# Kernel tuning notes

Measured on AMD Instinct MI355X. Metric: run time of the kernel, lower is better.

The kernel has to match this reference:

```python
import jax, jax.numpy as jnp
import numpy as np

D = 512          # sequence_dim
H = 8            # num_heads
DA = 64          # attn_dim per head
DV = 64          # linear_dim per head
NB = 4           # num_blocks
N = 1024         # max_seq_length + max_output_len + 1
B = 4
EPS = 1e-6


def setup_inputs() -> dict:
    key = jax.random.key(0)
    ks = jax.random.split(key, 8)
    sequence = jax.random.normal(ks[0], (B, N, D), dtype=jnp.float32)
    sequence_length = jax.random.randint(ks[1], (B,), 1, 1014)
    pos_embed = jax.random.normal(ks[2], (N, D), dtype=jnp.float32)  # nn.Embedding ~ N(0,1)
    w_uvqk = jax.random.normal(ks[3], (NB, D, 2 * H * DV + 2 * H * DA), dtype=jnp.float32) * 0.02
    w_o = jax.random.normal(ks[4], (NB, H * DV, D), dtype=jnp.float32) * 0.02
    b_o = jnp.zeros((NB, D), dtype=jnp.float32)
    ln1_g = jnp.ones((NB, D), dtype=jnp.float32)
    ln1_b = jnp.zeros((NB, D), dtype=jnp.float32)
    ln2_g = jnp.ones((NB, H * DV), dtype=jnp.float32)
    ln2_b = jnp.zeros((NB, H * DV), dtype=jnp.float32)
    pos_w = jax.random.normal(ks[5], (NB, 2 * N - 1), dtype=jnp.float32) * 0.02
    return {
        'sequence': sequence, 'sequence_length': sequence_length,
        'pos_embed': pos_embed, 'ln1_g': ln1_g, 'ln1_b': ln1_b,
        'w_uvqk': w_uvqk, 'ln2_g': ln2_g, 'ln2_b': ln2_b,
        'w_o': w_o, 'b_o': b_o, 'pos_w': pos_w,
    }


def _layer_norm(x, g, b):
    mu = jnp.mean(x, axis=-1, keepdims=True)
    var = jnp.mean(jnp.square(x - mu), axis=-1, keepdims=True)
    return (x - mu) * jax.lax.rsqrt(var + EPS) * g + b


def reference(sequence, sequence_length, pos_embed, ln1_g, ln1_b, w_uvqk,
              ln2_g, ln2_b, w_o, b_o, pos_w):
    # positional embedding + scale (inference: dropout = identity)
    x = sequence * jnp.asarray(np.sqrt(D), sequence.dtype) + pos_embed[None, :, :]
    # length mask (dense-padded equivalent of the jagged representation)
    mask = (jnp.arange(N)[None, :] < sequence_length[:, None]).astype(sequence.dtype)[..., None]
    x = x * mask
    # invalid_attn_mask = 1 - triu(ones, diag=1): causal incl. diagonal
    causal = jnp.tril(jnp.ones((N, N), sequence.dtype))
    # rel_pos_bias[i, j] = pos_w[j - i + N - 1]
    idx = jnp.arange(N)
    rel = idx[None, :] - idx[:, None] + (N - 1)  # (N, N) in [0, 2N-2]
    for l in range(NB):
        nx = _layer_norm(x, ln1_g[l], ln1_b[l])
        uvqk = jax.nn.silu(nx @ w_uvqk[l])  # (B, N, 2*H*DV + 2*H*DA)
        u, v, q, k = jnp.split(uvqk, [H * DV, 2 * H * DV, 2 * H * DV + H * DA], axis=-1)
        qh = q.reshape(x.shape[0], N, H, DA)
        kh = k.reshape(x.shape[0], N, H, DA)
        vh = v.reshape(x.shape[0], N, H, DV)
        qk = jnp.einsum('bnhd,bmhd->bhnm', qh, kh) + pos_w[l][rel][None, None]
        attn = jax.nn.silu(qk) * (causal / N)  # (B, H, N, N)
        av = jnp.einsum('bhnm,bmhd->bnhd', attn, vh).reshape(x.shape[0], N, H * DV)
        o_in = _layer_norm(av, ln2_g[l], ln2_b[l]) * u
        x = (x + o_in @ w_o[l] + b_o[l]) * mask  # mask = dense<->jagged roundtrip
    # output_embeddings[..., :D] then L2-normalize with clamped norm
    norm = jnp.linalg.norm(x, axis=-1, keepdims=True)
    return x / jnp.clip(norm, 1e-6, None)
```

## Files before the change

kernel.cpp:

```cpp
#include <hip/hip_runtime.h>
#include <math.h>
#include <stdint.h>

#define NN 1024
#define ROWS 4096
#define NBL 4

typedef _Float16 h8 __attribute__((ext_vector_type(8)));
typedef _Float16 h4 __attribute__((ext_vector_type(4)));
typedef float f4 __attribute__((ext_vector_type(4)));

__device__ __forceinline__ float fast_silu(float x) {
    float e = __builtin_amdgcn_exp2f(-1.4426950408889634f * x);
    return x * __builtin_amdgcn_rcpf(1.0f + e);
}

__device__ __forceinline__ void gl16(const void* gp, void* lp) {
    __builtin_amdgcn_global_load_lds(
        (const __attribute__((address_space(1))) uint32_t*)gp,
        (__attribute__((address_space(3))) uint32_t*)lp, 16, 0, 0);
}

__device__ __forceinline__ float wred(float s) {
    #pragma unroll
    for (int off = 1; off < 64; off <<= 1) s += __shfl_xor(s, off);
    return s;
}

__global__ __launch_bounds__(256) void k_transpose16(const float* __restrict__ wuvqk,
                                                     _Float16* __restrict__ wuT,
                                                     const float* __restrict__ wo,
                                                     _Float16* __restrict__ woT) {
    __shared__ _Float16 T[64][66];
    int z = blockIdx.z;
    const float* s; _Float16* d; int N;
    if (z < 4) { N = 2048; s = wuvqk + (size_t)z * 512 * 2048; d = wuT + (size_t)z * 2048 * 512; }
    else {
        if (blockIdx.x >= 8) return;
        N = 512; s = wo + (size_t)(z - 4) * 512 * 512; d = woT + (size_t)(z - 4) * 512 * 512;
    }
    int n0 = blockIdx.x << 6, k0 = blockIdx.y << 6;
    int tx = threadIdx.x & 63, ty = threadIdx.x >> 6;
    #pragma unroll
    for (int q = 0; q < 16; ++q)
        T[(q << 2) + ty][tx] = (_Float16)s[(size_t)(k0 + (q << 2) + ty) * N + n0 + tx];
    __syncthreads();
    #pragma unroll
    for (int q = 0; q < 16; ++q)
        d[(size_t)(n0 + (q << 2) + ty) * 512 + k0 + tx] = T[tx][(q << 2) + ty];
}

template<int MODE>
__global__ __launch_bounds__(256) void k_lnw(const float* __restrict__ X,
                                             const float* __restrict__ X2,
                                             const float* __restrict__ X3,
                                             const float* __restrict__ seq,
                                             const float* __restrict__ pos,
                                             const int* __restrict__ slen,
                                             const float* __restrict__ g,
                                             const float* __restrict__ bt,
                                             _Float16* __restrict__ O,
                                             const _Float16* __restrict__ U,
                                             float* __restrict__ Xw) {
    int tid = threadIdx.x;
    int w = tid >> 6, lane = tid & 63;
    int c = lane << 3;
    #pragma unroll
    for (int rr = 0; rr < 2; ++rr) {
        int row = (blockIdx.x << 3) + (w << 1) + rr;
        float v[8];
        if (MODE == 1) {
            int b = row >> 10, n = row & (NN - 1);
            float m = (n < slen[b]) ? 1.0f : 0.0f;
            const float4* sp = (const float4*)&seq[(size_t)row * 512 + c];
            const float4* pp = (const float4*)&pos[(size_t)n * 512 + c];
            const float SD = 22.627416997969522f;
            float4 s0 = sp[0], s1 = sp[1], p0 = pp[0], p1 = pp[1];
            v[0]=(s0.x*SD+p0.x)*m; v[1]=(s0.y*SD+p0.y)*m; v[2]=(s0.z*SD+p0.z)*m; v[3]=(s0.w*SD+p0.w)*m;
            v[4]=(s1.x*SD+p1.x)*m; v[5]=(s1.y*SD+p1.y)*m; v[6]=(s1.z*SD+p1.z)*m; v[7]=(s1.w*SD+p1.w)*m;
            float4 o0, o1;
            o0.x=v[0]; o0.y=v[1]; o0.z=v[2]; o0.w=v[3];
            o1.x=v[4]; o1.y=v[5]; o1.z=v[6]; o1.w=v[7];
            float4* xp = (float4*)&Xw[(size_t)row * 512 + c];
            xp[0] = o0; xp[1] = o1;
        } else {
            const float4* xp = (const float4*)&X[(size_t)row * 512 + c];
            float4 a = xp[0], b4 = xp[1];
            v[0]=a.x; v[1]=a.y; v[2]=a.z; v[3]=a.w; v[4]=b4.x; v[5]=b4.y; v[6]=b4.z; v[7]=b4.w;
            if (MODE == 2) {
                int nn = row & (NN - 1);
                if (nn >= 384) {
                    const float4* qp = (const float4*)&X2[(size_t)row * 512 + c];
                    float4 t0 = qp[0], t1 = qp[1];
                    v[0]+=t0.x; v[1]+=t0.y; v[2]+=t0.z; v[3]+=t0.w;
                    v[4]+=t1.x; v[5]+=t1.y; v[6]+=t1.z; v[7]+=t1.w;
                }
                if (nn >= 768) {
                    const float4* qp = (const float4*)&X3[(size_t)row * 512 + c];
                    float4 t0 = qp[0], t1 = qp[1];
                    v[0]+=t0.x; v[1]+=t0.y; v[2]+=t0.z; v[3]+=t0.w;
                    v[4]+=t1.x; v[5]+=t1.y; v[6]+=t1.z; v[7]+=t1.w;
                }
            }
        }
        float s = v[0]+v[1]+v[2]+v[3]+v[4]+v[5]+v[6]+v[7];
        s = wred(s);
        float mu = s * (1.0f / 512.0f);
        float ss = 0.0f;
        #pragma unroll
        for (int i = 0; i < 8; ++i) { float d = v[i] - mu; ss += d * d; }
        ss = wred(ss);
        float rs = rsqrtf(ss * (1.0f / 512.0f) + 1e-6f);

        const float4* gp = (const float4*)&g[c];
        const float4* bp = (const float4*)&bt[c];
        float4 g0 = gp[0], g1 = gp[1], b0 = bp[0], b1 = bp[1];
        float gg[8] = {g0.x,g0.y,g0.z,g0.w,g1.x,g1.y,g1.z,g1.w};
        float bb[8] = {b0.x,b0.y,b0.z,b0.w,b1.x,b1.y,b1.z,b1.w};
        float o[8];
        #pragma unroll
        for (int i = 0; i < 8; ++i) o[i] = (v[i] - mu) * rs * gg[i] + bb[i];
        if (MODE == 2) {
            h8 uu = *(const h8*)&U[(size_t)row * 2048 + c];
            #pragma unroll
            for (int i = 0; i < 8; ++i) o[i] *= (float)uu[i];
        }
        h8 oh;
        #pragma unroll
        for (int i = 0; i < 8; ++i) oh[i] = (_Float16)o[i];
        *(h8*)&O[(size_t)row * 512 + c] = oh;
    }
}

__global__ __launch_bounds__(256) void k_normw(float* __restrict__ X) {
    int tid = threadIdx.x;
    int w = tid >> 6, lane = tid & 63;
    int c = lane << 3;
    #pragma unroll
    for (int rr = 0; rr < 2; ++rr) {
        int row = (blockIdx.x << 3) + (w << 1) + rr;
        float4* xp = (float4*)&X[(size_t)row * 512 + c];
        float4 a = xp[0], b4 = xp[1];
        float ss = a.x*a.x + a.y*a.y + a.z*a.z + a.w*a.w +
                   b4.x*b4.x + b4.y*b4.y + b4.z*b4.z + b4.w*b4.w;
        ss = wred(ss);
        float sc = 1.0f / fmaxf(sqrtf(ss), 1e-6f);
        a.x*=sc; a.y*=sc; a.z*=sc; a.w*=sc; b4.x*=sc; b4.y*=sc; b4.z*=sc; b4.w*=sc;
        xp[0] = a; xp[1] = b4;
    }
}

template<int EPI, int BM, int BN, int WAVES, int WGR, int WGC>
__global__ __launch_bounds__(WAVES * 64) void k_gemm(const _Float16* __restrict__ A,
                                                     const _Float16* __restrict__ Bm,
                                                     _Float16* __restrict__ Cu,
                                                     _Float16* __restrict__ vT,
                                                     const float* __restrict__ bo,
                                                     const int* __restrict__ slen,
                                                     float* __restrict__ Xio) {
    constexpr int WR = BM / WGR / 16;
    constexpr int WC = BN / WGC / 16;
    constexpr int QA = BM * 8 / (WAVES * 64);
    constexpr int QB = BN * 8 / (WAVES * 64);
    __shared__ _Float16 smem[2 * 64 * (BM + BN)];
    _Float16* AsB = smem;
    _Float16* BsB = smem + 2 * BM * 64;
    int tid = threadIdx.x;
    int w = tid >> 6, lane = tid & 63;
    int t = lane & 15, gq = lane >> 4;
    int flat = blockIdx.y * gridDim.x + blockIdx.x;
    int cpx = (gridDim.x * gridDim.y) >> 3;
    int f2 = (flat & 7) * cpx + (flat >> 3);
    int bx = f2 % gridDim.x, by = f2 / gridDim.x;
    int row0 = by * BM, col0 = bx * BN;
    int wr = (w / WGC) * (BM / WGR), wc = (w % WGC) * (BN / WGC);

    f4 zero4 = {0.0f, 0.0f, 0.0f, 0.0f};
    f4 acc[WR][WC];
    #pragma unroll
    for (int i = 0; i < WR; ++i)
        #pragma unroll
        for (int j = 0; j < WC; ++j) acc[i][j] = zero4;

    auto stage = [&](int buf, int k0) {
        _Float16* As = AsB + buf * BM * 64;
        _Float16* Bs = BsB + buf * BN * 64;
        #pragma unroll
        for (int q = 0; q < QA; ++q) {
            int s = (q * WAVES + w) * 64 + lane;
            int r = s >> 3, cs = (s & 7) ^ (r & 7);
            gl16(A + (size_t)(row0 + r) * 512 + k0 + (cs << 3),
                 (char*)As + (size_t)(q * WAVES + w) * 1024);
        }
        #pragma unroll
        for (int q = 0; q < QB; ++q) {
            int s = (q * WAVES + w) * 64 + lane;
            int r = s >> 3, cs = (s & 7) ^ (r & 7);
            gl16(Bm + (size_t)(col0 + r) * 512 + k0 + (cs << 3),
                 (char*)Bs + (size_t)(q * WAVES + w) * 1024);
        }
    };

    stage(0, 0);
    int cur = 0;
    for (int k0 = 0; k0 < 512; k0 += 64) {
        __syncthreads();
        if (k0 + 64 < 512) stage(cur ^ 1, k0 + 64);
        const char* As = (const char*)(AsB + cur * BM * 64);
        const char* Bs = (const char*)(BsB + cur * BN * 64);
        h8 af[WR][2], bf[WC][2];
        #pragma unroll
        for (int i = 0; i < WR; ++i) {
            int rl = wr + (i << 4) + t;
            #pragma unroll
            for (int ks = 0; ks < 2; ++ks)
                af[i][ks] = *(const h8*)(As + rl * 128 + (((gq + (ks << 2)) ^ (rl & 7)) << 4));
        }
        #pragma unroll
        for (int j = 0; j < WC; ++j) {
            int nl = wc + (j << 4) + t;
            #pragma unroll
            for (int ks = 0; ks < 2; ++ks)
                bf[j][ks] = *(const h8*)(Bs + nl * 128 + (((gq + (ks << 2)) ^ (nl & 7)) << 4));
        }
        #pragma unroll
        for (int i = 0; i < WR; ++i)
            #pragma unroll
            for (int j = 0; j < WC; ++j) {
                acc[i][j] = __builtin_amdgcn_mfma_f32_16x16x32_f16(af[i][0], bf[j][0], acc[i][j], 0, 0, 0);
                acc[i][j] = __builtin_amdgcn_mfma_f32_16x16x32_f16(af[i][1], bf[j][1], acc[i][j], 0, 0, 0);
            }
        cur ^= 1;
    }

    if (EPI == 0) {
        _Float16* E = smem;
        bool vblk = (col0 >= 512 && col0 < 1024);
        __syncthreads();
        if (vblk) {
            #pragma unroll
            for (int i = 0; i < WR; ++i)
                #pragma unroll
                for (int j = 0; j < WC; ++j) {
                    int cl = wc + (j << 4) + t;
                    int rl = wr + (i << 4) + (gq << 2);
                    h4 pk;
                    #pragma unroll
                    for (int rr = 0; rr < 4; ++rr) pk[rr] = (_Float16)fast_silu(acc[i][j][rr]);
                    *(h4*)&E[cl * 136 + rl] = pk;
                }
        } else {
            #pragma unroll
            for (int i = 0; i < WR; ++i)
                #pragma unroll
                for (int j = 0; j < WC; ++j) {
                    int cl = wc + (j << 4) + t;
                    int rl = wr + (i << 4) + (gq << 2);
                    #pragma unroll
                    for (int rr = 0; rr < 4; ++rr)
                        E[(rl + rr) * 136 + cl] = (_Float16)fast_silu(acc[i][j][rr]);
                }
        }
        __syncthreads();
        constexpr int ITERS = 128 * 16 / (WAVES * 64);
        if (vblk) {
            int b = row0 >> 10;
            int n0l = row0 & 1023;
            #pragma unroll
            for (int it = 0; it < ITERS; ++it) {
                int dl = it * (WAVES * 4) + (tid >> 4);
                int cc = tid & 15;
                h8 vv = *(const h8*)&E[dl * 136 + (cc << 3)];
                int hh = (col0 + dl - 512) >> 6, dd = (col0 + dl - 512) & 63;
                *(h8*)&vT[((size_t)((b << 3) + hh) * 64 + dd) * 1024 + n0l + (cc << 3)] = vv;
            }
        } else {
            #pragma unroll
            for (int it = 0; it < ITERS; ++it) {
                int rl = it * (WAVES * 4) + (tid >> 4);
                int cc = tid & 15;
                h8 vv = *(const h8*)&E[rl * 136 + (cc << 3)];
                *(h8*)&Cu[(size_t)(row0 + rl) * 2048 + col0 + (cc << 3)] = vv;
            }
        }
    } else {
        #pragma unroll
        for (int i = 0; i < WR; ++i) {
            #pragma unroll
            for (int j = 0; j < WC; ++j) {
                int colf = col0 + wc + (j << 4) + t;
                int rowb = row0 + wr + (i << 4) + (gq << 2);
                int b = rowb >> 10;
                #pragma unroll
                for (int rr = 0; rr < 4; ++rr) {
                    int row = rowb + rr;
                    float m = ((row & 1023) < slen[b]) ? 1.0f : 0.0f;
                    size_t ix = (size_t)row * 512 + colf;
                    Xio[ix] = (Xio[ix] + acc[i][j][rr] + bo[colf]) * m;
                }
            }
        }
    }
}

__global__ __launch_bounds__(256) void k_attn(const _Float16* __restrict__ uvqk,
                                              const _Float16* __restrict__ vT,
                                              const float* __restrict__ posw,
                                              float* __restrict__ av0,
                                              float* __restrict__ av1,
                                              float* __restrict__ av2) {
    __shared__ _Float16 Ks[2][64 * 64];
    __shared__ _Float16 Vs[64 * 64];
    __shared__ _Float16 Ps[64 * 72];
    __shared__ float pws[2][128];
    int tid = threadIdx.x;
    int w = tid >> 6, lane = tid & 63;
    int t = lane & 15, gq = lane >> 4;
    int flat = blockIdx.x + 30 * (blockIdx.y + 8 * blockIdx.z);
    int f2 = (flat & 7) * 120 + (flat >> 3);
    int u = f2 % 30, h = (f2 / 30) & 7, b = f2 / 240;

    int nt, mlo, mhi;
    float* avout;
    if (u < 6) { nt = u; mlo = 0; mhi = nt; avout = av0; }
    else if (u < 18) {
        int p = u - 6; nt = 6 + (p >> 1);
        int c0 = (nt + 2) >> 1;
        if (p & 1) { mlo = c0; mhi = nt; avout = av1; }
        else       { mlo = 0;  mhi = c0 - 1; avout = av0; }
    } else {
        int p = u - 18; int third = p / 3; nt = 12 + third; int q3 = p - 3 * third;
        int c = nt + 1, c1 = (c + 2) / 3, c2 = (2 * c + 2) / 3;
        if (q3 == 0)      { mlo = 0;  mhi = c1 - 1; avout = av0; }
        else if (q3 == 1) { mlo = c1; mhi = c2 - 1; avout = av1; }
        else              { mlo = c2; mhi = nt;     avout = av2; }
    }
    int n0 = nt << 6;

    const _Float16* qbase = uvqk + (size_t)b * NN * 2048 + 1024 + h * 64;
    const _Float16* kbase = uvqk + (size_t)b * NN * 2048 + 1536 + h * 64;
    const _Float16* vbase = vT + (size_t)((b << 3) + h) * 64 * 1024;

    #pragma unroll
    for (int q = 0; q < 2; ++q) {
        int s = (((w << 1) + q) << 6) + lane;
        int r = s >> 3, cs = (s & 7) ^ (r & 7);
        gl16(qbase + (size_t)(n0 + r) * 2048 + (cs << 3),
             (char*)&Ks[1][0] + (size_t)(((w << 1) + q) << 6) * 16);
        gl16(kbase + (size_t)((mlo << 6) + r) * 2048 + (cs << 3),
             (char*)&Ks[0][0] + (size_t)(((w << 1) + q) << 6) * 16);
    }
    if (tid < 128) pws[0][tid] = posw[(mlo << 6) - n0 + tid + 960];
    __syncthreads();

    h8 aq[2];
    {
        int rl = (w << 4) + t;
        #pragma unroll
        for (int ks = 0; ks < 2; ++ks)
            aq[ks] = *(const h8*)((const char*)&Ks[1][0] + rl * 128 +
                                  (((gq + (ks << 2)) ^ (rl & 7)) << 4));
    }
    asm volatile("s_waitcnt lgkmcnt(0)" ::: "memory");
    __builtin_amdgcn_sched_barrier(0);
    __syncthreads();

    f4 zero4 = {0.0f, 0.0f, 0.0f, 0.0f};
    f4 avacc[4];
    #pragma unroll
    for (int j = 0; j < 4; ++j) avacc[j] = zero4;

    int cur = 0;
    for (int mt = mlo; mt <= mhi; ++mt) {
        int m0 = mt << 6;
        #pragma unroll
        for (int q = 0; q < 2; ++q) {
            int s = (((w << 1) + q) << 6) + lane;
            int r = s >> 3, cs = (s & 7) ^ (r & 7);
            gl16(vbase + (size_t)r * 1024 + m0 + (cs << 3),
                 (char*)&Vs[0] + (size_t)(((w << 1) + q) << 6) * 16);
        }
        int mt2 = (mt < mhi) ? mt + 1 : mt;
        #pragma unroll
        for (int q = 0; q < 2; ++q) {
            int s = (((w << 1) + q) << 6) + lane;
            int r = s >> 3, cs = (s & 7) ^ (r & 7);
            gl16(kbase + (size_t)((mt2 << 6) + r) * 2048 + (cs << 3),
                 (char*)&Ks[cur ^ 1][0] + (size_t)(((w << 1) + q) << 6) * 16);
        }
        if (tid < 128) pws[cur ^ 1][tid] = posw[(mt2 << 6) - n0 + tid + 960];

        f4 sacc[4];
        __builtin_amdgcn_s_setprio(1);
        #pragma unroll
        for (int i = 0; i < 4; ++i) {
            f4 binit;
            #pragma unroll
            for (int rr = 0; rr < 4; ++rr)
                binit[rr] = pws[cur][63 + (i << 4) + (gq << 2) + rr - ((w << 4) + t)];
            int ml = (i << 4) + t;
            h8 ak0 = *(const h8*)((const char*)&Ks[cur][0] + ml * 128 + (((gq + 0) ^ (ml & 7)) << 4));
            h8 ak1 = *(const h8*)((const char*)&Ks[cur][0] + ml * 128 + (((gq + 4) ^ (ml & 7)) << 4));
            sacc[i] = __builtin_amdgcn_mfma_f32_16x16x32_f16(ak0, aq[0], binit, 0, 0, 0);
            sacc[i] = __builtin_amdgcn_mfma_f32_16x16x32_f16(ak1, aq[1], sacc[i], 0, 0, 0);
        }
        __builtin_amdgcn_s_setprio(0);
        int nabs = n0 + (w << 4) + t;
        #pragma unroll
        for (int i = 0; i < 4; ++i) {
            int mb = m0 + (i << 4) + (gq << 2);
            h4 pk;
            #pragma unroll
            for (int rr = 0; rr < 4; ++rr) {
                float p = (mb + rr <= nabs) ? fast_silu(sacc[i][rr]) : 0.0f;
                pk[rr] = (_Float16)p;
            }
            *(h4*)((char*)Ps + ((w << 4) + t) * 144 + (i << 5) + (gq << 3)) = pk;
        }
        asm volatile("s_waitcnt lgkmcnt(0)" ::: "memory");
        asm volatile("s_waitcnt vmcnt(2)" ::: "memory");
        __builtin_amdgcn_s_barrier();
        __builtin_amdgcn_s_setprio(1);
        #pragma unroll
        for (int ks = 0; ks < 2; ++ks) {
            h8 pa = *(const h8*)((const char*)Ps + ((w << 4) + t) * 144 + (ks << 6) + (gq << 4));
            #pragma unroll
            for (int jt = 0; jt < 4; ++jt) {
                int dl = (jt << 4) + t;
                h8 bv = *(const h8*)((const char*)&Vs[0] + dl * 128 +
                                     (((gq + (ks << 2)) ^ (dl & 7)) << 4));
                avacc[jt] = __builtin_amdgcn_mfma_f32_16x16x32_f16(pa, bv, avacc[jt], 0, 0, 0);
            }
        }
        __builtin_amdgcn_s_setprio(0);
        __syncthreads();
        cur ^= 1;
    }

    #pragma unroll
    for (int jt = 0; jt < 4; ++jt) {
        #pragma unroll
        for (int rr = 0; rr < 4; ++rr) {
            int n = n0 + (w << 4) + (gq << 2) + rr;
            int d = (jt << 4) + t;
            avout[(size_t)(b * NN + n) * 512 + h * 64 + d] = avacc[jt][rr] * (1.0f / 1024.0f);
        }
    }
}

extern "C" void kernel_launch(void* const* d_in, const int* in_sizes, int n_in,
                              void* d_out, int out_size, void* d_ws, size_t ws_size,
                              hipStream_t stream) {
    const float* seq   = (const float*)d_in[0];
    const int*   slen  = (const int*)d_in[1];
    const float* pos   = (const float*)d_in[2];
    const float* ln1g  = (const float*)d_in[3];
    const float* ln1b  = (const float*)d_in[4];
    const float* wuvqk = (const float*)d_in[5];
    const float* ln2g  = (const float*)d_in[6];
    const float* ln2b  = (const float*)d_in[7];
    const float* wo    = (const float*)d_in[8];
    const float* bo    = (const float*)d_in[9];
    const float* posw  = (const float*)d_in[10];

    float* x = (float*)d_out;
    char* W = (char*)d_ws;
    _Float16* nx16   = (_Float16*)(W);
    _Float16* oin16  = (_Float16*)(W + (4u << 20));
    _Float16* uvqk16 = (_Float16*)(W + (8u << 20));
    _Float16* vT16   = (_Float16*)(W + (24u << 20));
    float*    av0    = (float*)   (W + (28u << 20));
    float*    av1    = (float*)   (W + (36u << 20));
    float*    av2    = (float*)   (W + (44u << 20));
    _Float16* wuT16  = (_Float16*)(W + (52u << 20));
    _Float16* woT16  = (_Float16*)(W + (60u << 20));

    k_transpose16<<<dim3(32, 8, 8), 256, 0, stream>>>(wuvqk, wuT16, wo, woT16);
    for (int l = 0; l < NBL; ++l) {
        if (l == 0)
            k_lnw<1><<<512, 256, 0, stream>>>(nullptr, nullptr, nullptr, seq, pos, slen,
                                              ln1g, ln1b, nx16, nullptr, x);
        else
            k_lnw<0><<<512, 256, 0, stream>>>(x, nullptr, nullptr, nullptr, nullptr, nullptr,
                                              ln1g + l * 512, ln1b + l * 512, nx16, nullptr, nullptr);
        k_gemm<0, 128, 128, 8, 2, 4><<<dim3(16, 32), 512, 0, stream>>>(
            nx16, wuT16 + (size_t)l * 2048 * 512, uvqk16, vT16, nullptr, nullptr, nullptr);
        k_attn<<<dim3(30, 8, NBL), 256, 0, stream>>>(uvqk16, vT16, posw + l * (2 * NN - 1),
                                                     av0, av1, av2);
        k_lnw<2><<<512, 256, 0, stream>>>(av0, av1, av2, nullptr, nullptr, nullptr,
                                          ln2g + l * 512, ln2b + l * 512, oin16, uvqk16, nullptr);
        k_gemm<1, 64, 32, 4, 2, 2><<<dim3(16, 64), 256, 0, stream>>>(
            oin16, woT16 + (size_t)l * 512 * 512, nullptr, nullptr, bo + l * 512, slen, x);
    }
    k_normw<<<512, 256, 0, stream>>>(x);
}
```

Before: 208.7 us.

## Fuse second layernorm and u-gating into output projection GEMM

```diff
diff --git a/kernel.cpp b/kernel.cpp
--- a/kernel.cpp
+++ b/kernel.cpp
@@ -52,15 +52,12 @@
 
 template<int MODE>
 __global__ __launch_bounds__(256) void k_lnw(const float* __restrict__ X,
-                                             const float* __restrict__ X2,
-                                             const float* __restrict__ X3,
                                              const float* __restrict__ seq,
                                              const float* __restrict__ pos,
                                              const int* __restrict__ slen,
                                              const float* __restrict__ g,
                                              const float* __restrict__ bt,
                                              _Float16* __restrict__ O,
-                                             const _Float16* __restrict__ U,
                                              float* __restrict__ Xw) {
     int tid = threadIdx.x;
     int w = tid >> 6, lane = tid & 63;
@@ -87,21 +84,6 @@
             const float4* xp = (const float4*)&X[(size_t)row * 512 + c];
             float4 a = xp[0], b4 = xp[1];
             v[0]=a.x; v[1]=a.y; v[2]=a.z; v[3]=a.w; v[4]=b4.x; v[5]=b4.y; v[6]=b4.z; v[7]=b4.w;
-            if (MODE == 2) {
-                int nn = row & (NN - 1);
-                if (nn >= 384) {
-                    const float4* qp = (const float4*)&X2[(size_t)row * 512 + c];
-                    float4 t0 = qp[0], t1 = qp[1];
-                    v[0]+=t0.x; v[1]+=t0.y; v[2]+=t0.z; v[3]+=t0.w;
-                    v[4]+=t1.x; v[5]+=t1.y; v[6]+=t1.z; v[7]+=t1.w;
-                }
-                if (nn >= 768) {
-                    const float4* qp = (const float4*)&X3[(size_t)row * 512 + c];
-                    float4 t0 = qp[0], t1 = qp[1];
-                    v[0]+=t0.x; v[1]+=t0.y; v[2]+=t0.z; v[3]+=t0.w;
-                    v[4]+=t1.x; v[5]+=t1.y; v[6]+=t1.z; v[7]+=t1.w;
-                }
-            }
         }
         float s = v[0]+v[1]+v[2]+v[3]+v[4]+v[5]+v[6]+v[7];
         s = wred(s);
@@ -117,17 +99,9 @@
         float4 g0 = gp[0], g1 = gp[1], b0 = bp[0], b1 = bp[1];
         float gg[8] = {g0.x,g0.y,g0.z,g0.w,g1.x,g1.y,g1.z,g1.w};
         float bb[8] = {b0.x,b0.y,b0.z,b0.w,b1.x,b1.y,b1.z,b1.w};
-        float o[8];
-        #pragma unroll
-        for (int i = 0; i < 8; ++i) o[i] = (v[i] - mu) * rs * gg[i] + bb[i];
-        if (MODE == 2) {
-            h8 uu = *(const h8*)&U[(size_t)row * 2048 + c];
-            #pragma unroll
-            for (int i = 0; i < 8; ++i) o[i] *= (float)uu[i];
-        }
         h8 oh;
         #pragma unroll
-        for (int i = 0; i < 8; ++i) oh[i] = (_Float16)o[i];
+        for (int i = 0; i < 8; ++i) oh[i] = (_Float16)((v[i] - mu) * rs * gg[i] + bb[i]);
         *(h8*)&O[(size_t)row * 512 + c] = oh;
     }
 }
@@ -150,18 +124,12 @@
     }
 }
 
-template<int EPI, int BM, int BN, int WAVES, int WGR, int WGC>
-__global__ __launch_bounds__(WAVES * 64) void k_gemm(const _Float16* __restrict__ A,
-                                                     const _Float16* __restrict__ Bm,
-                                                     _Float16* __restrict__ Cu,
-                                                     _Float16* __restrict__ vT,
-                                                     const float* __restrict__ bo,
-                                                     const int* __restrict__ slen,
-                                                     float* __restrict__ Xio) {
-    constexpr int WR = BM / WGR / 16;
-    constexpr int WC = BN / WGC / 16;
-    constexpr int QA = BM * 8 / (WAVES * 64);
-    constexpr int QB = BN * 8 / (WAVES * 64);
+__global__ __launch_bounds__(512) void k_gemm0(const _Float16* __restrict__ A,
+                                               const _Float16* __restrict__ Bm,
+                                               _Float16* __restrict__ Cu,
+                                               _Float16* __restrict__ vT) {
+    constexpr int BM = 128, BN = 128, WAVES = 8;
+    constexpr int QA = 2, QB = 2;
     __shared__ _Float16 smem[2 * 64 * (BM + BN)];
     _Float16* AsB = smem;
     _Float16* BsB = smem + 2 * BM * 64;
@@ -173,14 +141,14 @@
     int f2 = (flat & 7) * cpx + (flat >> 3);
     int bx = f2 % gridDim.x, by = f2 / gridDim.x;
     int row0 = by * BM, col0 = bx * BN;
-    int wr = (w / WGC) * (BM / WGR), wc = (w % WGC) * (BN / WGC);
+    int wr = (w >> 2) << 6, wc = (w & 3) << 5;
 
     f4 zero4 = {0.0f, 0.0f, 0.0f, 0.0f};
-    f4 acc[WR][WC];
-    #pragma unroll
-    for (int i = 0; i < WR; ++i)
-        #pragma unroll
-        for (int j = 0; j < WC; ++j) acc[i][j] = zero4;
+    f4 acc[4][2];
+    #pragma unroll
+    for (int i = 0; i < 4; ++i)
+        #pragma unroll
+        for (int j = 0; j < 2; ++j) acc[i][j] = zero4;
 
     auto stage = [&](int buf, int k0) {
         _Float16* As = AsB + buf * BM * 64;
@@ -208,97 +176,77 @@
         if (k0 + 64 < 512) stage(cur ^ 1, k0 + 64);
         const char* As = (const char*)(AsB + cur * BM * 64);
         const char* Bs = (const char*)(BsB + cur * BN * 64);
-        h8 af[WR][2], bf[WC][2];
-        #pragma unroll
-        for (int i = 0; i < WR; ++i) {
+        h8 af[4][2], bf[2][2];
+        #pragma unroll
+        for (int i = 0; i < 4; ++i) {
             int rl = wr + (i << 4) + t;
             #pragma unroll
             for (int ks = 0; ks < 2; ++ks)
                 af[i][ks] = *(const h8*)(As + rl * 128 + (((gq + (ks << 2)) ^ (rl & 7)) << 4));
         }
         #pragma unroll
-        for (int j = 0; j < WC; ++j) {
+        for (int j = 0; j < 2; ++j) {
             int nl = wc + (j << 4) + t;
             #pragma unroll
             for (int ks = 0; ks < 2; ++ks)
                 bf[j][ks] = *(const h8*)(Bs + nl * 128 + (((gq + (ks << 2)) ^ (nl & 7)) << 4));
         }
         #pragma unroll
-        for (int i = 0; i < WR; ++i)
-            #pragma unroll
-            for (int j = 0; j < WC; ++j) {
+        for (int i = 0; i < 4; ++i)
+            #pragma unroll
+            for (int j = 0; j < 2; ++j) {
                 acc[i][j] = __builtin_amdgcn_mfma_f32_16x16x32_f16(af[i][0], bf[j][0], acc[i][j], 0, 0, 0);
                 acc[i][j] = __builtin_amdgcn_mfma_f32_16x16x32_f16(af[i][1], bf[j][1], acc[i][j], 0, 0, 0);
             }
         cur ^= 1;
     }
 
-    if (EPI == 0) {
-        _Float16* E = smem;
-        bool vblk = (col0 >= 512 && col0 < 1024);
-        __syncthreads();
-        if (vblk) {
-            #pragma unroll
-            for (int i = 0; i < WR; ++i)
+    _Float16* E = smem;
+    bool vblk = (col0 >= 512 && col0 < 1024);
+    __syncthreads();
+    if (vblk) {
+        #pragma unroll
+        for (int i = 0; i < 4; ++i)
+            #pragma unroll
+            for (int j = 0; j < 2; ++j) {
+                int cl = wc + (j << 4) + t;
+                int rl = wr + (i << 4) + (gq << 2);
+                h4 pk;
                 #pragma unroll
-                for (int j = 0; j < WC; ++j) {
-                    int cl = wc + (j << 4) + t;
-                    int rl = wr + (i << 4) + (gq << 2);
-                    h4 pk;
-                    #pragma unroll
-                    for (int rr = 0; rr < 4; ++rr) pk[rr] = (_Float16)fast_silu(acc[i][j][rr]);
-                    *(h4*)&E[cl * 136 + rl] = pk;
-                }
-        } else {
-            #pragma unroll
-            for (int i = 0; i < WR; ++i)
+                for (int rr = 0; rr < 4; ++rr) pk[rr] = (_Float16)fast_silu(acc[i][j][rr]);
+                *(h4*)&E[cl * 136 + rl] = pk;
+            }
+    } else {
+        #pragma unroll
+        for (int i = 0; i < 4; ++i)
+            #pragma unroll
+            for (int j = 0; j < 2; ++j) {
+                int cl = wc + (j << 4) + t;
+                int rl = wr + (i << 4) + (gq << 2);
                 #pragma unroll
-                for (int j = 0; j < WC; ++j) {
-                    int cl = wc + (j << 4) + t;
-                    int rl = wr + (i << 4) + (gq << 2);
-                    #pragma unroll
-                    for (int rr = 0; rr < 4; ++rr)
-                        E[(rl + rr) * 136 + cl] = (_Float16)fast_silu(acc[i][j][rr]);
-                }
-        }
-        __syncthreads();
-        constexpr int ITERS = 128 * 16 / (WAVES * 64);
-        if (vblk) {
-            int b = row0 >> 10;
-            int n0l = row0 & 1023;
-            #pragma unroll
-            for (int it = 0; it < ITERS; ++it) {
-                int dl = it * (WAVES * 4) + (tid >> 4);
-                int cc = tid & 15;
-                h8 vv = *(const h8*)&E[dl * 136 + (cc << 3)];
-                int hh = (col0 + dl - 512) >> 6, dd = (col0 + dl - 512) & 63;
-                *(h8*)&vT[((size_t)((b << 3) + hh) * 64 + dd) * 1024 + n0l + (cc << 3)] = vv;
+                for (int rr = 0; rr < 4; ++rr)
+                    E[(rl + rr) * 136 + cl] = (_Float16)fast_silu(acc[i][j][rr]);
             }
-        } else {
-            #pragma unroll
-            for (int it = 0; it < ITERS; ++it) {
-                int rl = it * (WAVES * 4) + (tid >> 4);
-                int cc = tid & 15;
-                h8 vv = *(const h8*)&E[rl * 136 + (cc << 3)];
-                *(h8*)&Cu[(size_t)(row0 + rl) * 2048 + col0 + (cc << 3)] = vv;
-            }
+    }
+    __syncthreads();
+    if (vblk) {
+        int b = row0 >> 10;
+        int n0l = row0 & 1023;
+        #pragma unroll
+        for (int it = 0; it < 4; ++it) {
+            int dl = (it << 5) + (tid >> 4);
+            int cc = tid & 15;
+            h8 vv = *(const h8*)&E[dl * 136 + (cc << 3)];
+            int hh = (col0 + dl - 512) >> 6, dd = (col0 + dl - 512) & 63;
+            *(h8*)&vT[((size_t)((b << 3) + hh) * 64 + dd) * 1024 + n0l + (cc << 3)] = vv;
         }
     } else {
         #pragma unroll
-        for (int i = 0; i < WR; ++i) {
-            #pragma unroll
-            for (int j = 0; j < WC; ++j) {
-                int colf = col0 + wc + (j << 4) + t;
-                int rowb = row0 + wr + (i << 4) + (gq << 2);
-                int b = rowb >> 10;
-                #pragma unroll
-                for (int rr = 0; rr < 4; ++rr) {
-                    int row = rowb + rr;
-                    float m = ((row & 1023) < slen[b]) ? 1.0f : 0.0f;
-                    size_t ix = (size_t)row * 512 + colf;
-                    Xio[ix] = (Xio[ix] + acc[i][j][rr] + bo[colf]) * m;
-                }
-            }
+        for (int it = 0; it < 4; ++it) {
+            int rl = (it << 5) + (tid >> 4);
+            int cc = tid & 15;
+            h8 vv = *(const h8*)&E[rl * 136 + (cc << 3)];
+            *(h8*)&Cu[(size_t)(row0 + rl) * 2048 + col0 + (cc << 3)] = vv;
         }
     }
 }
@@ -312,7 +260,7 @@
     __shared__ _Float16 Ks[2][64 * 64];
     __shared__ _Float16 Vs[64 * 64];
     __shared__ _Float16 Ps[64 * 72];
-    __shared__ float pws[2][128];
+    __shared__ float pwall[448];
     int tid = threadIdx.x;
     int w = tid >> 6, lane = tid & 63;
     int t = lane & 15, gq = lane >> 4;
@@ -346,11 +294,15 @@
         int s = (((w << 1) + q) << 6) + lane;
         int r = s >> 3, cs = (s & 7) ^ (r & 7);
         gl16(qbase + (size_t)(n0 + r) * 2048 + (cs << 3),
-             (char*)&Ks[1][0] + (size_t)(((w << 1) + q) << 6) * 16);
+             (char*)&Ks[1][0] + (((w << 1) + q) << 10));
         gl16(kbase + (size_t)((mlo << 6) + r) * 2048 + (cs << 3),
-             (char*)&Ks[0][0] + (size_t)(((w << 1) + q) << 6) * 16);
-    }
-    if (tid < 128) pws[0][tid] = posw[(mlo << 6) - n0 + tid + 960];
+             (char*)&Ks[0][0] + (((w << 1) + q) << 10));
+    }
+    {
+        int span = ((mhi - mlo) << 6) + 128;
+        int base2 = (mlo << 6) - n0 + 960;
+        for (int idx = tid; idx < span; idx += 256) pwall[idx] = posw[base2 + idx];
+    }
     __syncthreads();
 
     h8 aq[2];
@@ -378,7 +330,7 @@
             int s = (((w << 1) + q) << 6) + lane;
             int r = s >> 3, cs = (s & 7) ^ (r & 7);
             gl16(vbase + (size_t)r * 1024 + m0 + (cs << 3),
-                 (char*)&Vs[0] + (size_t)(((w << 1) + q) << 6) * 16);
+                 (char*)&Vs[0] + (((w << 1) + q) << 10));
         }
         int mt2 = (mt < mhi) ? mt + 1 : mt;
         #pragma unroll
@@ -386,18 +338,17 @@
             int s = (((w << 1) + q) << 6) + lane;
             int r = s >> 3, cs = (s & 7) ^ (r & 7);
             gl16(kbase + (size_t)((mt2 << 6) + r) * 2048 + (cs << 3),
-                 (char*)&Ks[cur ^ 1][0] + (size_t)(((w << 1) + q) << 6) * 16);
-        }
-        if (tid < 128) pws[cur ^ 1][tid] = posw[(mt2 << 6) - n0 + tid + 960];
+                 (char*)&Ks[cur ^ 1][0] + (((w << 1) + q) << 10));
+        }
 
         f4 sacc[4];
         __builtin_amdgcn_s_setprio(1);
         #pragma unroll
         for (int i = 0; i < 4; ++i) {
             f4 binit;
-            #pragma unroll
-            for (int rr = 0; rr < 4; ++rr)
-                binit[rr] = pws[cur][63 + (i << 4) + (gq << 2) + rr - ((w << 4) + t)];
+            int pb = ((mt - mlo) << 6) + 63 + (i << 4) + (gq << 2) - ((w << 4) + t);
+            #pragma unroll
+            for (int rr = 0; rr < 4; ++rr) binit[rr] = pwall[pb + rr];
             int ml = (i << 4) + t;
             h8 ak0 = *(const h8*)((const char*)&Ks[cur][0] + ml * 128 + (((gq + 0) ^ (ml & 7)) << 4));
             h8 ak1 = *(const h8*)((const char*)&Ks[cur][0] + ml * 128 + (((gq + 4) ^ (ml & 7)) << 4));
@@ -444,6 +395,126 @@
             int n = n0 + (w << 4) + (gq << 2) + rr;
             int d = (jt << 4) + t;
             avout[(size_t)(b * NN + n) * 512 + h * 64 + d] = avacc[jt][rr] * (1.0f / 1024.0f);
+        }
+    }
+}
+
+__global__ __launch_bounds__(256) void k_og(const float* __restrict__ av0,
+                                            const float* __restrict__ av1,
+                                            const float* __restrict__ av2,
+                                            const float* __restrict__ g,
+                                            const float* __restrict__ bt,
+                                            const _Float16* __restrict__ U,
+                                            const _Float16* __restrict__ Bm,
+                                            const float* __restrict__ bo,
+                                            const int* __restrict__ slen,
+                                            float* __restrict__ Xio) {
+    __shared__ _Float16 smem[16 * 512 + 2 * 128 * 64];
+    _Float16* As = smem;
+    _Float16* BsB = smem + 16 * 512;
+    int tid = threadIdx.x;
+    int w = tid >> 6, lane = tid & 63;
+    int t = lane & 15, gq = lane >> 4;
+    int flat = blockIdx.y * gridDim.x + blockIdx.x;
+    int cpx = (gridDim.x * gridDim.y) >> 3;
+    int f2 = (flat & 7) * cpx + (flat >> 3);
+    int bx = f2 % gridDim.x, by = f2 / gridDim.x;
+    int row0 = by * 16, col0 = bx * 128;
+
+    auto stageB = [&](int buf, int k0) {
+        _Float16* Bs = BsB + buf * (128 * 64);
+        #pragma unroll
+        for (int q = 0; q < 4; ++q) {
+            int s = ((q << 2) + w) * 64 + lane;
+            int r = s >> 3, cs = (s & 7) ^ (r & 7);
+            gl16(Bm + (size_t)(col0 + r) * 512 + k0 + (cs << 3),
+                 (char*)Bs + (size_t)((q << 2) + w) * 1024);
+        }
+    };
+    stageB(0, 0);
+
+    int c = lane << 3;
+    #pragma unroll
+    for (int rr = 0; rr < 4; ++rr) {
+        int r = (w << 2) + rr;
+        int row = row0 + r;
+        const float4* xp = (const float4*)&av0[(size_t)row * 512 + c];
+        float4 a = xp[0], b4 = xp[1];
+        float v[8] = {a.x, a.y, a.z, a.w, b4.x, b4.y, b4.z, b4.w};
+        int nn = row & (NN - 1);
+        if (nn >= 384) {
+            const float4* qp = (const float4*)&av1[(size_t)row * 512 + c];
+            float4 t0 = qp[0], t1 = qp[1];
+            v[0]+=t0.x; v[1]+=t0.y; v[2]+=t0.z; v[3]+=t0.w;
+            v[4]+=t1.x; v[5]+=t1.y; v[6]+=t1.z; v[7]+=t1.w;
+        }
+        if (nn >= 768) {
+            const float4* qp = (const float4*)&av2[(size_t)row * 512 + c];
+            float4 t0 = qp[0], t1 = qp[1];
+            v[0]+=t0.x; v[1]+=t0.y; v[2]+=t0.z; v[3]+=t0.w;
+            v[4]+=t1.x; v[5]+=t1.y; v[6]+=t1.z; v[7]+=t1.w;
+        }
+        float s = v[0]+v[1]+v[2]+v[3]+v[4]+v[5]+v[6]+v[7];
+        s = wred(s);
+        float mu = s * (1.0f / 512.0f);
+        float ss = 0.0f;
+        #pragma unroll
+        for (int i = 0; i < 8; ++i) { float d = v[i] - mu; ss += d * d; }
+        ss = wred(ss);
+        float rs = rsqrtf(ss * (1.0f / 512.0f) + 1e-6f);
+
+        const float4* gp = (const float4*)&g[c];
+        const float4* bp = (const float4*)&bt[c];
+        float4 g0 = gp[0], g1 = gp[1], b0 = bp[0], b1 = bp[1];
+        float gg[8] = {g0.x,g0.y,g0.z,g0.w,g1.x,g1.y,g1.z,g1.w};
+        float bb[8] = {b0.x,b0.y,b0.z,b0.w,b1.x,b1.y,b1.z,b1.w};
+        h8 uu = *(const h8*)&U[(size_t)row * 2048 + c];
+        h8 oh;
+        #pragma unroll
+        for (int i = 0; i < 8; ++i)
+            oh[i] = (_Float16)(((v[i] - mu) * rs * gg[i] + bb[i]) * (float)uu[i]);
+        *(h8*)((char*)As + ((lane >> 3) << 11) + r * 128 + (((lane & 7) ^ (r & 7)) << 4)) = oh;
+    }
+
+    f4 zero4 = {0.0f, 0.0f, 0.0f, 0.0f};
+    f4 acc[2];
+    acc[0] = zero4; acc[1] = zero4;
+    int cur = 0;
+    for (int k0 = 0; k0 < 512; k0 += 64) {
+        __syncthreads();
+        if (k0 + 64 < 512) stageB(cur ^ 1, k0 + 64);
+        const char* Asg = (const char*)As + ((k0 >> 6) << 11);
+        const char* Bs = (const char*)(BsB + cur * (128 * 64));
+        h8 af[2], bf[2][2];
+        #pragma unroll
+        for (int ks = 0; ks < 2; ++ks)
+            af[ks] = *(const h8*)(Asg + t * 128 + (((gq + (ks << 2)) ^ (t & 7)) << 4));
+        #pragma unroll
+        for (int j = 0; j < 2; ++j) {
+            int nl = (w << 5) + (j << 4) + t;
+            #pragma unroll
+            for (int ks = 0; ks < 2; ++ks)
+                bf[j][ks] = *(const h8*)(Bs + nl * 128 + (((gq + (ks << 2)) ^ (nl & 7)) << 4));
+        }
+        #pragma unroll
+        for (int j = 0; j < 2; ++j) {
+            acc[j] = __builtin_amdgcn_mfma_f32_16x16x32_f16(af[0], bf[j][0], acc[j], 0, 0, 0);
+            acc[j] = __builtin_amdgcn_mfma_f32_16x16x32_f16(af[1], bf[j][1], acc[j], 0, 0, 0);
+        }
+        cur ^= 1;
+    }
+
+    int b = row0 >> 10;
+    #pragma unroll
+    for (int j = 0; j < 2; ++j) {
+        int colf = col0 + (w << 5) + (j << 4) + t;
+        float bov = bo[colf];
+        #pragma unroll
+        for (int rr = 0; rr < 4; ++rr) {
+            int row = row0 + (gq << 2) + rr;
+            float m = ((row & 1023) < slen[b]) ? 1.0f : 0.0f;
+            size_t ix = (size_t)row * 512 + colf;
+            Xio[ix] = (Xio[ix] + acc[j][rr] + bov) * m;
         }
     }
 }
@@ -466,31 +537,28 @@
     float* x = (float*)d_out;
     char* W = (char*)d_ws;
     _Float16* nx16   = (_Float16*)(W);
-    _Float16* oin16  = (_Float16*)(W + (4u << 20));
-    _Float16* uvqk16 = (_Float16*)(W + (8u << 20));
-    _Float16* vT16   = (_Float16*)(W + (24u << 20));
-    float*    av0    = (float*)   (W + (28u << 20));
-    float*    av1    = (float*)   (W + (36u << 20));
-    float*    av2    = (float*)   (W + (44u << 20));
-    _Float16* wuT16  = (_Float16*)(W + (52u << 20));
-    _Float16* woT16  = (_Float16*)(W + (60u << 20));
+    _Float16* uvqk16 = (_Float16*)(W + (4u << 20));
+    _Float16* vT16   = (_Float16*)(W + (20u << 20));
+    float*    av0    = (float*)   (W + (24u << 20));
+    float*    av1    = (float*)   (W + (32u << 20));
+    float*    av2    = (float*)   (W + (40u << 20));
+    _Float16* wuT16  = (_Float16*)(W + (48u << 20));
+    _Float16* woT16  = (_Float16*)(W + (56u << 20));
 
     k_transpose16<<<dim3(32, 8, 8), 256, 0, stream>>>(wuvqk, wuT16, wo, woT16);
     for (int l = 0; l < NBL; ++l) {
         if (l == 0)
-            k_lnw<1><<<512, 256, 0, stream>>>(nullptr, nullptr, nullptr, seq, pos, slen,
-                                              ln1g, ln1b, nx16, nullptr, x);
+            k_lnw<1><<<512, 256, 0, stream>>>(nullptr, seq, pos, slen, ln1g, ln1b, nx16, x);
         else
-            k_lnw<0><<<512, 256, 0, stream>>>(x, nullptr, nullptr, nullptr, nullptr, nullptr,
-                                              ln1g + l * 512, ln1b + l * 512, nx16, nullptr, nullptr);
-        k_gemm<0, 128, 128, 8, 2, 4><<<dim3(16, 32), 512, 0, stream>>>(
-            nx16, wuT16 + (size_t)l * 2048 * 512, uvqk16, vT16, nullptr, nullptr, nullptr);
+            k_lnw<0><<<512, 256, 0, stream>>>(x, nullptr, nullptr, nullptr,
+                                              ln1g + l * 512, ln1b + l * 512, nx16, nullptr);
+        k_gemm0<<<dim3(16, 32), 512, 0, stream>>>(nx16, wuT16 + (size_t)l * 2048 * 512,
+                                                  uvqk16, vT16);
         k_attn<<<dim3(30, 8, NBL), 256, 0, stream>>>(uvqk16, vT16, posw + l * (2 * NN - 1),
                                                      av0, av1, av2);
-        k_lnw<2><<<512, 256, 0, stream>>>(av0, av1, av2, nullptr, nullptr, nullptr,
-                                          ln2g + l * 512, ln2b + l * 512, oin16, uvqk16, nullptr);
-        k_gemm<1, 64, 32, 4, 2, 2><<<dim3(16, 64), 256, 0, stream>>>(
-            oin16, woT16 + (size_t)l * 512 * 512, nullptr, nullptr, bo + l * 512, slen, x);
+        k_og<<<dim3(4, 256), 256, 0, stream>>>(av0, av1, av2, ln2g + l * 512, ln2b + l * 512,
+                                               uvqk16, woT16 + (size_t)l * 512 * 512,
+                                               bo + l * 512, slen, x);
     }
     k_normw<<<512, 256, 0, stream>>>(x);
 }
```

Measured after the change: 227.6 us. 1.09x slower.

## Enlarge attention query tile to 128 rows with 8 waves per block

Applied to the files above, without the earlier changes.

```diff
diff --git a/kernel.cpp b/kernel.cpp
--- a/kernel.cpp
+++ b/kernel.cpp
@@ -303,7 +303,7 @@
     }
 }
 
-__global__ __launch_bounds__(256) void k_attn(const _Float16* __restrict__ uvqk,
+__global__ __launch_bounds__(512) void k_attn(const _Float16* __restrict__ uvqk,
                                               const _Float16* __restrict__ vT,
                                               const float* __restrict__ posw,
                                               float* __restrict__ av0,
@@ -311,31 +311,31 @@
                                               float* __restrict__ av2) {
     __shared__ _Float16 Ks[2][64 * 64];
     __shared__ _Float16 Vs[64 * 64];
-    __shared__ _Float16 Ps[64 * 72];
-    __shared__ float pws[2][128];
+    __shared__ _Float16 Ps[128 * 72];
+    __shared__ float pws[2][192];
     int tid = threadIdx.x;
     int w = tid >> 6, lane = tid & 63;
     int t = lane & 15, gq = lane >> 4;
-    int flat = blockIdx.x + 30 * (blockIdx.y + 8 * blockIdx.z);
-    int f2 = (flat & 7) * 120 + (flat >> 3);
-    int u = f2 % 30, h = (f2 / 30) & 7, b = f2 / 240;
-
-    int nt, mlo, mhi;
+    int flat = blockIdx.x + 15 * (blockIdx.y + 8 * blockIdx.z);
+    int f2 = (flat & 7) * 60 + (flat >> 3);
+    int u = f2 % 15, h = (f2 / 15) & 7, b = f2 / 120;
+
+    int qt, mlo, mhi;
     float* avout;
-    if (u < 6) { nt = u; mlo = 0; mhi = nt; avout = av0; }
-    else if (u < 18) {
-        int p = u - 6; nt = 6 + (p >> 1);
-        int c0 = (nt + 2) >> 1;
-        if (p & 1) { mlo = c0; mhi = nt; avout = av1; }
+    if (u < 3) { qt = u; mlo = 0; mhi = 2 * qt + 1; avout = av0; }
+    else if (u < 9) {
+        int p = u - 3; qt = 3 + (p >> 1);
+        int c0 = qt + 1;
+        if (p & 1) { mlo = c0; mhi = 2 * qt + 1; avout = av1; }
         else       { mlo = 0;  mhi = c0 - 1; avout = av0; }
     } else {
-        int p = u - 18; int third = p / 3; nt = 12 + third; int q3 = p - 3 * third;
-        int c = nt + 1, c1 = (c + 2) / 3, c2 = (2 * c + 2) / 3;
+        int p = u - 9; int third = p / 3; qt = 6 + third; int q3 = p - 3 * third;
+        int c = 2 * qt + 2, c1 = (c + 2) / 3, c2 = (2 * c + 2) / 3;
         if (q3 == 0)      { mlo = 0;  mhi = c1 - 1; avout = av0; }
         else if (q3 == 1) { mlo = c1; mhi = c2 - 1; avout = av1; }
-        else              { mlo = c2; mhi = nt;     avout = av2; }
-    }
-    int n0 = nt << 6;
+        else              { mlo = c2; mhi = 2 * qt + 1; avout = av2; }
+    }
+    int n0 = qt << 7;
 
     const _Float16* qbase = uvqk + (size_t)b * NN * 2048 + 1024 + h * 64;
     const _Float16* kbase = uvqk + (size_t)b * NN * 2048 + 1536 + h * 64;
@@ -346,11 +346,15 @@
         int s = (((w << 1) + q) << 6) + lane;
         int r = s >> 3, cs = (s & 7) ^ (r & 7);
         gl16(qbase + (size_t)(n0 + r) * 2048 + (cs << 3),
-             (char*)&Ks[1][0] + (size_t)(((w << 1) + q) << 6) * 16);
+             (char*)Ps + (((w << 1) + q) << 10));
+    }
+    {
+        int s = (w << 6) + lane;
+        int r = s >> 3, cs = (s & 7) ^ (r & 7);
         gl16(kbase + (size_t)((mlo << 6) + r) * 2048 + (cs << 3),
-             (char*)&Ks[0][0] + (size_t)(((w << 1) + q) << 6) * 16);
-    }
-    if (tid < 128) pws[0][tid] = posw[(mlo << 6) - n0 + tid + 960];
+             (char*)&Ks[0][0] + (w << 10));
+    }
+    if (tid < 192) pws[0][tid] = posw[(mlo << 6) - n0 + tid + 896];
     __syncthreads();
 
     h8 aq[2];
@@ -358,7 +362,7 @@
         int rl = (w << 4) + t;
         #pragma unroll
         for (int ks = 0; ks < 2; ++ks)
-            aq[ks] = *(const h8*)((const char*)&Ks[1][0] + rl * 128 +
+            aq[ks] = *(const h8*)((const char*)Ps + rl * 128 +
                                   (((gq + (ks << 2)) ^ (rl & 7)) << 4));
     }
     asm volatile("s_waitcnt lgkmcnt(0)" ::: "memory");
@@ -373,22 +377,20 @@
     int cur = 0;
     for (int mt = mlo; mt <= mhi; ++mt) {
         int m0 = mt << 6;
-        #pragma unroll
-        for (int q = 0; q < 2; ++q) {
-            int s = (((w << 1) + q) << 6) + lane;
+        {
+            int s = (w << 6) + lane;
             int r = s >> 3, cs = (s & 7) ^ (r & 7);
             gl16(vbase + (size_t)r * 1024 + m0 + (cs << 3),
-                 (char*)&Vs[0] + (size_t)(((w << 1) + q) << 6) * 16);
+                 (char*)&Vs[0] + (w << 10));
         }
         int mt2 = (mt < mhi) ? mt + 1 : mt;
-        #pragma unroll
-        for (int q = 0; q < 2; ++q) {
-            int s = (((w << 1) + q) << 6) + lane;
+        {
+            int s = (w << 6) + lane;
             int r = s >> 3, cs = (s & 7) ^ (r & 7);
             gl16(kbase + (size_t)((mt2 << 6) + r) * 2048 + (cs << 3),
-                 (char*)&Ks[cur ^ 1][0] + (size_t)(((w << 1) + q) << 6) * 16);
-        }
-        if (tid < 128) pws[cur ^ 1][tid] = posw[(mt2 << 6) - n0 + tid + 960];
+                 (char*)&Ks[cur ^ 1][0] + (w << 10));
+        }
+        if (tid < 192) pws[cur ^ 1][tid] = posw[(mt2 << 6) - n0 + tid + 896];
 
         f4 sacc[4];
         __builtin_amdgcn_s_setprio(1);
@@ -397,7 +399,7 @@
             f4 binit;
             #pragma unroll
             for (int rr = 0; rr < 4; ++rr)
-                binit[rr] = pws[cur][63 + (i << 4) + (gq << 2) + rr - ((w << 4) + t)];
+                binit[rr] = pws[cur][127 + (i << 4) + (gq << 2) + rr - ((w << 4) + t)];
             int ml = (i << 4) + t;
             h8 ak0 = *(const h8*)((const char*)&Ks[cur][0] + ml * 128 + (((gq + 0) ^ (ml & 7)) << 4));
             h8 ak1 = *(const h8*)((const char*)&Ks[cur][0] + ml * 128 + (((gq + 4) ^ (ml & 7)) << 4));
@@ -418,7 +420,7 @@
             *(h4*)((char*)Ps + ((w << 4) + t) * 144 + (i << 5) + (gq << 3)) = pk;
         }
         asm volatile("s_waitcnt lgkmcnt(0)" ::: "memory");
-        asm volatile("s_waitcnt vmcnt(2)" ::: "memory");
+        asm volatile("s_waitcnt vmcnt(1)" ::: "memory");
         __builtin_amdgcn_s_barrier();
         __builtin_amdgcn_s_setprio(1);
         #pragma unroll
@@ -485,7 +487,7 @@
                                               ln1g + l * 512, ln1b + l * 512, nx16, nullptr, nullptr);
         k_gemm<0, 128, 128, 8, 2, 4><<<dim3(16, 32), 512, 0, stream>>>(
             nx16, wuT16 + (size_t)l * 2048 * 512, uvqk16, vT16, nullptr, nullptr, nullptr);
-        k_attn<<<dim3(30, 8, NBL), 256, 0, stream>>>(uvqk16, vT16, posw + l * (2 * NN - 1),
+        k_attn<<<dim3(15, 8, NBL), 512, 0, stream>>>(uvqk16, vT16, posw + l * (2 * NN - 1),
                                                      av0, av1, av2);
         k_lnw<2><<<512, 256, 0, stream>>>(av0, av1, av2, nullptr, nullptr, nullptr,
                                           ln2g + l * 512, ln2b + l * 512, oin16, uvqk16, nullptr);
```

New measurement: 205.1 us. Within noise of the previous version (-1.7%).
